# Performance work log

Hardware: AMD Instinct MI355X
Metric: run time of the kernel (lower is better)

Reference implementation:

```python
import jax, jax.numpy as jnp
import numpy as np

HIDDEN = 1024
HEADS = 16
HEAD_DIM = HIDDEN // HEADS  # 64
LOCAL = (128, 128)
ROPE_MAX_POS = LOCAL[0] + LOCAL[1]  # 256 (local attention branch)
ROPE_BASE = 10000.0


def make_rope_cache(max_len, dim, base):
    positions = jnp.arange(max_len, dtype=jnp.float32)
    theta = 1.0 / base ** (jnp.arange(0, dim, 2, dtype=jnp.float32) / dim)
    angles = jnp.einsum('i,j->ij', positions, theta)
    return jnp.stack([jnp.cos(angles), jnp.sin(angles)], axis=-1)  # (max_len, dim//2, 2)


def apply_rope(x, cache):
    # x: (B, S, H, D); cache: (max_pos, D//2, 2)
    S = x.shape[1]
    pos = jnp.arange(S) % cache.shape[0]
    rc = cache[pos][None, :, None, :, :]  # (1, S, 1, D//2, 2)
    xr = x.reshape(*x.shape[:-1], -1, 2)
    x0, x1 = xr[..., 0], xr[..., 1]
    c, s = rc[..., 0], rc[..., 1]
    out = jnp.stack([x0 * c - x1 * s, x1 * c + x0 * s], axis=-1)
    return out.reshape(x.shape)


def sliding_window_mask(S, window, dtype):
    rel = jnp.arange(S)[:, None] - jnp.arange(S)[None, :]
    inside = (rel >= -window[0]) & (rel <= window[1])
    return jnp.where(inside, jnp.zeros((), dtype), -jnp.inf)[None, None]  # (1,1,S,S)


def setup_inputs() -> dict:
    key = jax.random.key(0)
    k1, k2, k3, k4, k5 = jax.random.split(key, 5)
    B, S = 2, 2048
    hidden_states = jax.random.normal(k1, (B, S, HIDDEN), dtype=jnp.float32)
    Wqkv_kernel = jax.random.normal(k2, (HIDDEN, 3 * HIDDEN), dtype=jnp.float32) / np.sqrt(HIDDEN)
    Wqkv_bias = jnp.zeros((3 * HIDDEN,), dtype=jnp.float32)
    Wo_kernel = jax.random.normal(k3, (HIDDEN, HIDDEN), dtype=jnp.float32) / np.sqrt(HIDDEN)
    Wo_bias = jnp.zeros((HIDDEN,), dtype=jnp.float32)
    rope_cache = make_rope_cache(ROPE_MAX_POS, HEAD_DIM, ROPE_BASE)
    return {
        'hidden_states': hidden_states,
        'Wqkv_kernel': Wqkv_kernel,
        'Wqkv_bias': Wqkv_bias,
        'Wo_kernel': Wo_kernel,
        'Wo_bias': Wo_bias,
        'rope_cache': rope_cache,
    }


def reference(hidden_states, Wqkv_kernel, Wqkv_bias, Wo_kernel, Wo_bias, rope_cache):
    B, S, _ = hidden_states.shape
    qkv = hidden_states @ Wqkv_kernel + Wqkv_bias  # (B,S,3*HIDDEN)
    qkv = qkv.reshape(B, S, 3, HEADS, HEAD_DIM)
    q = qkv[:, :, 0]  # (B,S,H,D)
    k = qkv[:, :, 1]
    v = qkv[:, :, 2]
    q = apply_rope(q, rope_cache)
    k = apply_rope(k, rope_cache)
    # to (B,H,S,D)
    q = jnp.transpose(q, (0, 2, 1, 3))
    k = jnp.transpose(k, (0, 2, 1, 3))
    v = jnp.transpose(v, (0, 2, 1, 3))
    scale = jnp.sqrt(jnp.float32(HEAD_DIM))
    scores = jnp.einsum('bhqd,bhkd->bhqk', q, k) / scale
    mask = sliding_window_mask(S, LOCAL, scores.dtype)
    probs = jax.nn.softmax(scores + mask, axis=-1)
    out = jnp.einsum('bhqk,bhkd->bqhd', probs, v).reshape(B, S, HIDDEN)
    out = out @ Wo_kernel + Wo_bias
    return out
```

## Files before the change

### kernel.cpp

```cpp
#include <hip/hip_runtime.h>
#include <hip/hip_bf16.h>

typedef __bf16 bf16x8 __attribute__((ext_vector_type(8)));
typedef __bf16 bf16x4 __attribute__((ext_vector_type(4)));
typedef float f32x4 __attribute__((ext_vector_type(4)));

#define SLEN 2048
#define NHEADS 16
#define HDIM 64

__global__ __launch_bounds__(256) void cast_f32_bf16(const float* __restrict__ in,
                                                     __bf16* __restrict__ out, int n4) {
    int i = blockIdx.x * 256 + threadIdx.x;
    if (i < n4) {
        float4 v = reinterpret_cast<const float4*>(in)[i];
        bf16x4 o = { (__bf16)v.x, (__bf16)v.y, (__bf16)v.z, (__bf16)v.w };
        reinterpret_cast<bf16x4*>(out)[i] = o;
    }
}

__global__ __launch_bounds__(256) void transpose_cast(const float* __restrict__ W,
                                                      __bf16* __restrict__ Wt,
                                                      int K, int N) {
    __shared__ float tile[32][33];
    int n0 = blockIdx.x * 32, k0 = blockIdx.y * 32;
    int tx = threadIdx.x, ty = threadIdx.y;
    #pragma unroll
    for (int i = ty; i < 32; i += 8)
        tile[i][tx] = W[(size_t)(k0 + i) * N + n0 + tx];
    __syncthreads();
    #pragma unroll
    for (int i = ty; i < 32; i += 8)
        Wt[(size_t)(n0 + i) * K + k0 + tx] = (__bf16)tile[tx][i];
}

__global__ __launch_bounds__(256) void gemm_bt(const __bf16* __restrict__ A,
                                               const __bf16* __restrict__ Bt,
                                               const float* __restrict__ bias,
                                               float* __restrict__ Cf,
                                               __bf16* __restrict__ Cq,
                                               __bf16* __restrict__ Ck,
                                               __bf16* __restrict__ Cv,
                                               int M, int N, int K, int epi) {
    __shared__ __align__(16) __bf16 As[128 * 40];
    __shared__ __align__(16) __bf16 Bs[128 * 40];

    int nb = N >> 7;
    int bx = blockIdx.x % nb;
    int by = blockIdx.x / nb;
    int row0 = by * 128, col0 = bx * 128;

    int tid = threadIdx.x;
    int wave = tid >> 6, lane = tid & 63;
    int quad = lane >> 4, lrow = lane & 15;
    int wm = wave >> 1, wn = wave & 1;

    int r1 = tid >> 2;
    int kk = (tid & 3) * 8;
    const __bf16* Aptr = A + (size_t)(row0 + r1) * K + kk;
    const __bf16* Bptr = Bt + (size_t)(col0 + r1) * K + kk;

    f32x4 acc[4][4];
    f32x4 zero = {0.f, 0.f, 0.f, 0.f};
    #pragma unroll
    for (int i = 0; i < 4; i++)
        #pragma unroll
        for (int j = 0; j < 4; j++) acc[i][j] = zero;

    for (int k0 = 0; k0 < K; k0 += 32) {
        bf16x8 a0 = *reinterpret_cast<const bf16x8*>(Aptr + k0);
        bf16x8 a1 = *reinterpret_cast<const bf16x8*>(Aptr + (size_t)64 * K + k0);
        bf16x8 b0 = *reinterpret_cast<const bf16x8*>(Bptr + k0);
        bf16x8 b1 = *reinterpret_cast<const bf16x8*>(Bptr + (size_t)64 * K + k0);
        __syncthreads();
        *reinterpret_cast<bf16x8*>(&As[r1 * 40 + kk]) = a0;
        *reinterpret_cast<bf16x8*>(&As[(r1 + 64) * 40 + kk]) = a1;
        *reinterpret_cast<bf16x8*>(&Bs[r1 * 40 + kk]) = b0;
        *reinterpret_cast<bf16x8*>(&Bs[(r1 + 64) * 40 + kk]) = b1;
        __syncthreads();

        bf16x8 af[4], bfr[4];
        #pragma unroll
        for (int i = 0; i < 4; i++)
            af[i] = *reinterpret_cast<const bf16x8*>(&As[(wm * 64 + i * 16 + lrow) * 40 + quad * 8]);
        #pragma unroll
        for (int j = 0; j < 4; j++)
            bfr[j] = *reinterpret_cast<const bf16x8*>(&Bs[(wn * 64 + j * 16 + lrow) * 40 + quad * 8]);
        #pragma unroll
        for (int i = 0; i < 4; i++)
            #pragma unroll
            for (int j = 0; j < 4; j++)
                acc[i][j] = __builtin_amdgcn_mfma_f32_16x16x32_bf16(af[i], bfr[j], acc[i][j], 0, 0, 0);
    }

    #pragma unroll
    for (int i = 0; i < 4; i++) {
        int rowb = row0 + wm * 64 + i * 16 + quad * 4;
        #pragma unroll
        for (int j = 0; j < 4; j++) {
            int col = col0 + wn * 64 + j * 16 + lrow;
            float bsv = bias[col];
            #pragma unroll
            for (int r = 0; r < 4; r++) {
                int row = rowb + r;
                float v = acc[i][j][r] + bsv;
                if (epi == 0) {
                    Cf[(size_t)row * N + col] = v;
                } else {
                    int part = col >> 10;
                    int h = (col >> 6) & 15;
                    int d = col & 63;
                    int b = row >> 11;
                    int s = row & 2047;
                    __bf16* dst = (part == 0) ? Cq : ((part == 1) ? Ck : Cv);
                    dst[((size_t)(b * NHEADS + h) * SLEN + s) * HDIM + d] = (__bf16)v;
                }
            }
        }
    }
}

__global__ __launch_bounds__(256) void rope_kernel(__bf16* __restrict__ Q,
                                                   __bf16* __restrict__ K,
                                                   const float* __restrict__ rope) {
    int idx = blockIdx.x * 256 + threadIdx.x;
    int p = idx & 31;
    int s = (idx >> 5) & 2047;
    int bh = idx >> 16;
    size_t off = ((size_t)bh * SLEN + s) * HDIM + 2 * p;
    int pos = s & 255;
    float c = rope[(pos * 32 + p) * 2];
    float sn = rope[(pos * 32 + p) * 2 + 1];
    float q0 = (float)Q[off], q1 = (float)Q[off + 1];
    Q[off]     = (__bf16)(q0 * c - q1 * sn);
    Q[off + 1] = (__bf16)(q1 * c + q0 * sn);
    float k0 = (float)K[off], k1 = (float)K[off + 1];
    K[off]     = (__bf16)(k0 * c - k1 * sn);
    K[off + 1] = (__bf16)(k1 * c + k0 * sn);
}

__global__ __launch_bounds__(256) void attn_kernel(const __bf16* __restrict__ Q,
                                                   const __bf16* __restrict__ Kt,
                                                   const __bf16* __restrict__ V,
                                                   __bf16* __restrict__ O) {
    __shared__ __align__(16) __bf16 Vt[64][40];
    __shared__ __align__(16) __bf16 Pl[4][16][40];

    int qt = blockIdx.x & 31;
    int bh = blockIdx.x >> 5;
    int q0 = qt * 64;
    const __bf16* Qbh = Q + (size_t)bh * SLEN * HDIM;
    const __bf16* Kbh = Kt + (size_t)bh * SLEN * HDIM;
    const __bf16* Vbh = V + (size_t)bh * SLEN * HDIM;

    int tid = threadIdx.x;
    int wave = tid >> 6, lane = tid & 63;
    int quad = lane >> 4, lrow = lane & 15;
    int wq0 = q0 + wave * 16;

    bf16x8 qa0 = *reinterpret_cast<const bf16x8*>(Qbh + (size_t)(wq0 + lrow) * HDIM + quad * 8);
    bf16x8 qa1 = *reinterpret_cast<const bf16x8*>(Qbh + (size_t)(wq0 + lrow) * HDIM + 32 + quad * 8);

    f32x4 zero = {0.f, 0.f, 0.f, 0.f};
    f32x4 acc[4];
    #pragma unroll
    for (int t = 0; t < 4; t++) acc[t] = zero;
    float m_i[4], l_i[4];
    #pragma unroll
    for (int r = 0; r < 4; r++) { m_i[r] = -1e30f; l_i[r] = 0.f; }

    int kstart = q0 - 128; if (kstart < 0) kstart = 0;
    int kend = q0 + 63 + 128 + 1; if (kend > SLEN) kend = SLEN;

    for (int kc = kstart; kc < kend; kc += 32) {
        __syncthreads();
        {
            int keyl = tid >> 3;
            int db = (tid & 7) * 8;
            bf16x8 vv = *reinterpret_cast<const bf16x8*>(Vbh + (size_t)(kc + keyl) * HDIM + db);
            #pragma unroll
            for (int i = 0; i < 8; i++) Vt[db + i][keyl] = vv[i];
        }
        __syncthreads();

        f32x4 c0 = zero, c1 = zero;
        {
            const __bf16* krow0 = Kbh + (size_t)(kc + lrow) * HDIM;
            const __bf16* krow1 = Kbh + (size_t)(kc + 16 + lrow) * HDIM;
            bf16x8 kb0a = *reinterpret_cast<const bf16x8*>(krow0 + quad * 8);
            bf16x8 kb0b = *reinterpret_cast<const bf16x8*>(krow0 + 32 + quad * 8);
            bf16x8 kb1a = *reinterpret_cast<const bf16x8*>(krow1 + quad * 8);
            bf16x8 kb1b = *reinterpret_cast<const bf16x8*>(krow1 + 32 + quad * 8);
            c0 = __builtin_amdgcn_mfma_f32_16x16x32_bf16(qa0, kb0a, c0, 0, 0, 0);
            c0 = __builtin_amdgcn_mfma_f32_16x16x32_bf16(qa1, kb0b, c0, 0, 0, 0);
            c1 = __builtin_amdgcn_mfma_f32_16x16x32_bf16(qa0, kb1a, c1, 0, 0, 0);
            c1 = __builtin_amdgcn_mfma_f32_16x16x32_bf16(qa1, kb1b, c1, 0, 0, 0);
        }

        #pragma unroll
        for (int r = 0; r < 4; r++) {
            int q = wq0 + quad * 4 + r;
            int key0 = kc + lrow;
            int key1 = kc + 16 + lrow;
            bool v0 = (key0 >= q - 128) && (key0 <= q + 128);
            bool v1 = (key1 >= q - 128) && (key1 <= q + 128);
            float s0 = v0 ? c0[r] * 0.125f : -1e30f;
            float s1 = v1 ? c1[r] * 0.125f : -1e30f;
            float rm = fmaxf(s0, s1);
            #pragma unroll
            for (int off = 1; off < 16; off <<= 1) rm = fmaxf(rm, __shfl_xor(rm, off, 64));
            float mnew = fmaxf(m_i[r], rm);
            float alpha = __expf(m_i[r] - mnew);
            float p0 = v0 ? __expf(s0 - mnew) : 0.0f;
            float p1 = v1 ? __expf(s1 - mnew) : 0.0f;
            float rs = p0 + p1;
            #pragma unroll
            for (int off = 1; off < 16; off <<= 1) rs += __shfl_xor(rs, off, 64);
            l_i[r] = l_i[r] * alpha + rs;
            m_i[r] = mnew;
            #pragma unroll
            for (int t = 0; t < 4; t++) acc[t][r] *= alpha;
            Pl[wave][quad * 4 + r][lrow] = (__bf16)p0;
            Pl[wave][quad * 4 + r][16 + lrow] = (__bf16)p1;
        }
        asm volatile("s_waitcnt lgkmcnt(0)" ::: "memory");

        bf16x8 ap = *reinterpret_cast<const bf16x8*>(&Pl[wave][lrow][quad * 8]);
        #pragma unroll
        for (int t = 0; t < 4; t++) {
            bf16x8 bv = *reinterpret_cast<const bf16x8*>(&Vt[t * 16 + lrow][quad * 8]);
            acc[t] = __builtin_amdgcn_mfma_f32_16x16x32_bf16(ap, bv, acc[t], 0, 0, 0);
        }
    }

    int b = bh >> 4, h = bh & 15;
    #pragma unroll
    for (int r = 0; r < 4; r++) {
        int stok = q0 + wave * 16 + quad * 4 + r;
        float inv = 1.0f / l_i[r];
        size_t base = ((size_t)b * SLEN + stok) * 1024 + h * HDIM;
        #pragma unroll
        for (int t = 0; t < 4; t++) {
            O[base + t * 16 + lrow] = (__bf16)(acc[t][r] * inv);
        }
    }
}

extern "C" void kernel_launch(void* const* d_in, const int* in_sizes, int n_in,
                              void* d_out, int out_size, void* d_ws, size_t ws_size,
                              hipStream_t stream) {
    const float* hidden = (const float*)d_in[0];
    const float* Wqkv   = (const float*)d_in[1];
    const float* bqkv   = (const float*)d_in[2];
    const float* Wo     = (const float*)d_in[3];
    const float* bo     = (const float*)d_in[4];
    const float* rope   = (const float*)d_in[5];
    float* out = (float*)d_out;

    char* ws = (char*)d_ws;
    __bf16* A1  = (__bf16*)(ws);
    __bf16* Wt  = (__bf16*)(ws + 8388608);
    __bf16* Wot = (__bf16*)(ws + 14680064);
    __bf16* Qb  = (__bf16*)(ws + 16777216);
    __bf16* Kb  = (__bf16*)(ws + 25165824);
    __bf16* Vb  = (__bf16*)(ws + 33554432);
    __bf16* AO  = (__bf16*)(ws + 41943040);

    cast_f32_bf16<<<4096, 256, 0, stream>>>(hidden, A1, 1048576);
    transpose_cast<<<dim3(96, 32), dim3(32, 8), 0, stream>>>(Wqkv, Wt, 1024, 3072);
    transpose_cast<<<dim3(32, 32), dim3(32, 8), 0, stream>>>(Wo, Wot, 1024, 1024);

    gemm_bt<<<32 * 24, 256, 0, stream>>>(A1, Wt, bqkv, nullptr, Qb, Kb, Vb,
                                         4096, 3072, 1024, 1);
    rope_kernel<<<8192, 256, 0, stream>>>(Qb, Kb, rope);
    attn_kernel<<<2 * 16 * 32, 256, 0, stream>>>(Qb, Kb, Vb, AO);
    gemm_bt<<<32 * 8, 256, 0, stream>>>(AO, Wot, bo, out, nullptr, nullptr, nullptr,
                                        4096, 1024, 1024, 0);
}
```

Before: 205.6 us.

## Fuse RoPE into QKV GEMM epilogue, async LDS loads, widen attention key chunks

Removes the standalone RoPE kernel by applying the rotation in the QKV GEMM epilogue, using a lane shuffle to fetch the paired element. This saves a full read and write pass over Q and K. The GEMM now loads tiles with global_load_lds direct-to-LDS copies into an XOR-swizzled unpadded layout instead of staging through registers. The attention kernel processes 64 keys per iteration instead of 32, which halves the barrier and softmax-reduction overhead per key but raises register and LDS use.

```diff
diff --git a/kernel.cpp b/kernel.cpp
--- a/kernel.cpp
+++ b/kernel.cpp
@@ -8,6 +8,12 @@
 #define SLEN 2048
 #define NHEADS 16
 #define HDIM 64
+
+__device__ __forceinline__ void async_copy16(const __bf16* g, void* l) {
+    __builtin_amdgcn_global_load_lds(
+        (const __attribute__((address_space(1))) void*)g,
+        (__attribute__((address_space(3))) void*)l, 16, 0, 0);
+}
 
 __global__ __launch_bounds__(256) void cast_f32_bf16(const float* __restrict__ in,
                                                      __bf16* __restrict__ out, int n4) {
@@ -37,13 +43,14 @@
 __global__ __launch_bounds__(256) void gemm_bt(const __bf16* __restrict__ A,
                                                const __bf16* __restrict__ Bt,
                                                const float* __restrict__ bias,
+                                               const float* __restrict__ rope,
                                                float* __restrict__ Cf,
                                                __bf16* __restrict__ Cq,
                                                __bf16* __restrict__ Ck,
                                                __bf16* __restrict__ Cv,
                                                int M, int N, int K, int epi) {
-    __shared__ __align__(16) __bf16 As[128 * 40];
-    __shared__ __align__(16) __bf16 Bs[128 * 40];
+    __shared__ __align__(16) __bf16 As[128 * 32];
+    __shared__ __align__(16) __bf16 Bs[128 * 32];
 
     int nb = N >> 7;
     int bx = blockIdx.x % nb;
@@ -57,8 +64,11 @@
 
     int r1 = tid >> 2;
     int kk = (tid & 3) * 8;
-    const __bf16* Aptr = A + (size_t)(row0 + r1) * K + kk;
-    const __bf16* Bptr = Bt + (size_t)(col0 + r1) * K + kk;
+    int kg = kk ^ (((r1 >> 1) & 3) * 8);
+    const __bf16* Ap = A + (size_t)(row0 + r1) * K + kg;
+    const __bf16* Bp = Bt + (size_t)(col0 + r1) * K + kg;
+    char* as_lo = (char*)As + wave * 1024;
+    char* bs_lo = (char*)Bs + wave * 1024;
 
     f32x4 acc[4][4];
     f32x4 zero = {0.f, 0.f, 0.f, 0.f};
@@ -67,25 +77,23 @@
         #pragma unroll
         for (int j = 0; j < 4; j++) acc[i][j] = zero;
 
+    int sA = (quad ^ ((lrow >> 1) & 3)) * 8;
+
     for (int k0 = 0; k0 < K; k0 += 32) {
-        bf16x8 a0 = *reinterpret_cast<const bf16x8*>(Aptr + k0);
-        bf16x8 a1 = *reinterpret_cast<const bf16x8*>(Aptr + (size_t)64 * K + k0);
-        bf16x8 b0 = *reinterpret_cast<const bf16x8*>(Bptr + k0);
-        bf16x8 b1 = *reinterpret_cast<const bf16x8*>(Bptr + (size_t)64 * K + k0);
-        __syncthreads();
-        *reinterpret_cast<bf16x8*>(&As[r1 * 40 + kk]) = a0;
-        *reinterpret_cast<bf16x8*>(&As[(r1 + 64) * 40 + kk]) = a1;
-        *reinterpret_cast<bf16x8*>(&Bs[r1 * 40 + kk]) = b0;
-        *reinterpret_cast<bf16x8*>(&Bs[(r1 + 64) * 40 + kk]) = b1;
+        __syncthreads();
+        async_copy16(Ap + k0, as_lo);
+        async_copy16(Ap + (size_t)64 * K + k0, as_lo + 4096);
+        async_copy16(Bp + k0, bs_lo);
+        async_copy16(Bp + (size_t)64 * K + k0, bs_lo + 4096);
         __syncthreads();
 
         bf16x8 af[4], bfr[4];
         #pragma unroll
         for (int i = 0; i < 4; i++)
-            af[i] = *reinterpret_cast<const bf16x8*>(&As[(wm * 64 + i * 16 + lrow) * 40 + quad * 8]);
+            af[i] = *reinterpret_cast<const bf16x8*>(&As[(wm * 64 + i * 16 + lrow) * 32 + sA]);
         #pragma unroll
         for (int j = 0; j < 4; j++)
-            bfr[j] = *reinterpret_cast<const bf16x8*>(&Bs[(wn * 64 + j * 16 + lrow) * 40 + quad * 8]);
+            bfr[j] = *reinterpret_cast<const bf16x8*>(&Bs[(wn * 64 + j * 16 + lrow) * 32 + sA]);
         #pragma unroll
         for (int i = 0; i < 4; i++)
             #pragma unroll
@@ -93,6 +101,8 @@
                 acc[i][j] = __builtin_amdgcn_mfma_f32_16x16x32_bf16(af[i], bfr[j], acc[i][j], 0, 0, 0);
     }
 
+    int part = col0 >> 10;
+    bool do_rope = (epi == 1) && (part < 2);
     #pragma unroll
     for (int i = 0; i < 4; i++) {
         int rowb = row0 + wm * 64 + i * 16 + quad * 4;
@@ -100,16 +110,23 @@
         for (int j = 0; j < 4; j++) {
             int col = col0 + wn * 64 + j * 16 + lrow;
             float bsv = bias[col];
+            int d = col & 63;
             #pragma unroll
             for (int r = 0; r < 4; r++) {
                 int row = rowb + r;
                 float v = acc[i][j][r] + bsv;
+                if (do_rope) {
+                    int pos = row & 255;
+                    int p = d >> 1;
+                    float c  = rope[(pos * 32 + p) * 2];
+                    float sn = rope[(pos * 32 + p) * 2 + 1];
+                    float other = __shfl_xor(v, 1, 64);
+                    v = (d & 1) ? fmaf(v, c, other * sn) : fmaf(v, c, -other * sn);
+                }
                 if (epi == 0) {
                     Cf[(size_t)row * N + col] = v;
                 } else {
-                    int part = col >> 10;
                     int h = (col >> 6) & 15;
-                    int d = col & 63;
                     int b = row >> 11;
                     int s = row & 2047;
                     __bf16* dst = (part == 0) ? Cq : ((part == 1) ? Ck : Cv);
@@ -120,31 +137,12 @@
     }
 }
 
-__global__ __launch_bounds__(256) void rope_kernel(__bf16* __restrict__ Q,
-                                                   __bf16* __restrict__ K,
-                                                   const float* __restrict__ rope) {
-    int idx = blockIdx.x * 256 + threadIdx.x;
-    int p = idx & 31;
-    int s = (idx >> 5) & 2047;
-    int bh = idx >> 16;
-    size_t off = ((size_t)bh * SLEN + s) * HDIM + 2 * p;
-    int pos = s & 255;
-    float c = rope[(pos * 32 + p) * 2];
-    float sn = rope[(pos * 32 + p) * 2 + 1];
-    float q0 = (float)Q[off], q1 = (float)Q[off + 1];
-    Q[off]     = (__bf16)(q0 * c - q1 * sn);
-    Q[off + 1] = (__bf16)(q1 * c + q0 * sn);
-    float k0 = (float)K[off], k1 = (float)K[off + 1];
-    K[off]     = (__bf16)(k0 * c - k1 * sn);
-    K[off + 1] = (__bf16)(k1 * c + k0 * sn);
-}
-
 __global__ __launch_bounds__(256) void attn_kernel(const __bf16* __restrict__ Q,
                                                    const __bf16* __restrict__ Kt,
                                                    const __bf16* __restrict__ V,
                                                    __bf16* __restrict__ O) {
-    __shared__ __align__(16) __bf16 Vt[64][40];
-    __shared__ __align__(16) __bf16 Pl[4][16][40];
+    __shared__ __align__(16) __bf16 Vt[64][72];
+    __shared__ __align__(16) __bf16 Pl[4][16][72];
 
     int qt = blockIdx.x & 31;
     int bh = blockIdx.x >> 5;
@@ -172,64 +170,75 @@
     int kstart = q0 - 128; if (kstart < 0) kstart = 0;
     int kend = q0 + 63 + 128 + 1; if (kend > SLEN) kend = SLEN;
 
-    for (int kc = kstart; kc < kend; kc += 32) {
+    for (int kc = kstart; kc < kend; kc += 64) {
         __syncthreads();
         {
-            int keyl = tid >> 3;
-            int db = (tid & 7) * 8;
-            bf16x8 vv = *reinterpret_cast<const bf16x8*>(Vbh + (size_t)(kc + keyl) * HDIM + db);
-            #pragma unroll
-            for (int i = 0; i < 8; i++) Vt[db + i][keyl] = vv[i];
-        }
-        __syncthreads();
-
-        f32x4 c0 = zero, c1 = zero;
-        {
-            const __bf16* krow0 = Kbh + (size_t)(kc + lrow) * HDIM;
-            const __bf16* krow1 = Kbh + (size_t)(kc + 16 + lrow) * HDIM;
-            bf16x8 kb0a = *reinterpret_cast<const bf16x8*>(krow0 + quad * 8);
-            bf16x8 kb0b = *reinterpret_cast<const bf16x8*>(krow0 + 32 + quad * 8);
-            bf16x8 kb1a = *reinterpret_cast<const bf16x8*>(krow1 + quad * 8);
-            bf16x8 kb1b = *reinterpret_cast<const bf16x8*>(krow1 + 32 + quad * 8);
-            c0 = __builtin_amdgcn_mfma_f32_16x16x32_bf16(qa0, kb0a, c0, 0, 0, 0);
-            c0 = __builtin_amdgcn_mfma_f32_16x16x32_bf16(qa1, kb0b, c0, 0, 0, 0);
-            c1 = __builtin_amdgcn_mfma_f32_16x16x32_bf16(qa0, kb1a, c1, 0, 0, 0);
-            c1 = __builtin_amdgcn_mfma_f32_16x16x32_bf16(qa1, kb1b, c1, 0, 0, 0);
+            int keyl = tid >> 2;
+            int db = (tid & 3) * 16;
+            const __bf16* vp = Vbh + (size_t)(kc + keyl) * HDIM + db;
+            bf16x8 v0 = *reinterpret_cast<const bf16x8*>(vp);
+            bf16x8 v1 = *reinterpret_cast<const bf16x8*>(vp + 8);
+            #pragma unroll
+            for (int i = 0; i < 8; i++) {
+                Vt[db + i][keyl] = v0[i];
+                Vt[db + 8 + i][keyl] = v1[i];
+            }
+        }
+        __syncthreads();
+
+        f32x4 cs[4];
+        #pragma unroll
+        for (int sub = 0; sub < 4; sub++) {
+            cs[sub] = zero;
+            const __bf16* krow = Kbh + (size_t)(kc + sub * 16 + lrow) * HDIM;
+            bf16x8 kba = *reinterpret_cast<const bf16x8*>(krow + quad * 8);
+            bf16x8 kbb = *reinterpret_cast<const bf16x8*>(krow + 32 + quad * 8);
+            cs[sub] = __builtin_amdgcn_mfma_f32_16x16x32_bf16(qa0, kba, cs[sub], 0, 0, 0);
+            cs[sub] = __builtin_amdgcn_mfma_f32_16x16x32_bf16(qa1, kbb, cs[sub], 0, 0, 0);
         }
 
         #pragma unroll
         for (int r = 0; r < 4; r++) {
             int q = wq0 + quad * 4 + r;
-            int key0 = kc + lrow;
-            int key1 = kc + 16 + lrow;
-            bool v0 = (key0 >= q - 128) && (key0 <= q + 128);
-            bool v1 = (key1 >= q - 128) && (key1 <= q + 128);
-            float s0 = v0 ? c0[r] * 0.125f : -1e30f;
-            float s1 = v1 ? c1[r] * 0.125f : -1e30f;
-            float rm = fmaxf(s0, s1);
+            float sc[4];
+            bool vd[4];
+            #pragma unroll
+            for (int sub = 0; sub < 4; sub++) {
+                int key = kc + sub * 16 + lrow;
+                vd[sub] = (key >= q - 128) && (key <= q + 128);
+                sc[sub] = vd[sub] ? cs[sub][r] * 0.125f : -1e30f;
+            }
+            float rm = fmaxf(fmaxf(sc[0], sc[1]), fmaxf(sc[2], sc[3]));
             #pragma unroll
             for (int off = 1; off < 16; off <<= 1) rm = fmaxf(rm, __shfl_xor(rm, off, 64));
             float mnew = fmaxf(m_i[r], rm);
             float alpha = __expf(m_i[r] - mnew);
-            float p0 = v0 ? __expf(s0 - mnew) : 0.0f;
-            float p1 = v1 ? __expf(s1 - mnew) : 0.0f;
-            float rs = p0 + p1;
+            float p[4], rs = 0.f;
+            #pragma unroll
+            for (int sub = 0; sub < 4; sub++) {
+                p[sub] = vd[sub] ? __expf(sc[sub] - mnew) : 0.0f;
+                rs += p[sub];
+            }
             #pragma unroll
             for (int off = 1; off < 16; off <<= 1) rs += __shfl_xor(rs, off, 64);
             l_i[r] = l_i[r] * alpha + rs;
             m_i[r] = mnew;
             #pragma unroll
             for (int t = 0; t < 4; t++) acc[t][r] *= alpha;
-            Pl[wave][quad * 4 + r][lrow] = (__bf16)p0;
-            Pl[wave][quad * 4 + r][16 + lrow] = (__bf16)p1;
+            #pragma unroll
+            for (int sub = 0; sub < 4; sub++)
+                Pl[wave][quad * 4 + r][sub * 16 + lrow] = (__bf16)p[sub];
         }
         asm volatile("s_waitcnt lgkmcnt(0)" ::: "memory");
 
-        bf16x8 ap = *reinterpret_cast<const bf16x8*>(&Pl[wave][lrow][quad * 8]);
+        bf16x8 ap0 = *reinterpret_cast<const bf16x8*>(&Pl[wave][lrow][quad * 8]);
+        bf16x8 ap1 = *reinterpret_cast<const bf16x8*>(&Pl[wave][lrow][32 + quad * 8]);
         #pragma unroll
         for (int t = 0; t < 4; t++) {
-            bf16x8 bv = *reinterpret_cast<const bf16x8*>(&Vt[t * 16 + lrow][quad * 8]);
-            acc[t] = __builtin_amdgcn_mfma_f32_16x16x32_bf16(ap, bv, acc[t], 0, 0, 0);
+            bf16x8 bv0 = *reinterpret_cast<const bf16x8*>(&Vt[t * 16 + lrow][quad * 8]);
+            bf16x8 bv1 = *reinterpret_cast<const bf16x8*>(&Vt[t * 16 + lrow][32 + quad * 8]);
+            acc[t] = __builtin_amdgcn_mfma_f32_16x16x32_bf16(ap0, bv0, acc[t], 0, 0, 0);
+            acc[t] = __builtin_amdgcn_mfma_f32_16x16x32_bf16(ap1, bv1, acc[t], 0, 0, 0);
         }
     }
 
@@ -270,10 +279,9 @@
     transpose_cast<<<dim3(96, 32), dim3(32, 8), 0, stream>>>(Wqkv, Wt, 1024, 3072);
     transpose_cast<<<dim3(32, 32), dim3(32, 8), 0, stream>>>(Wo, Wot, 1024, 1024);
 
-    gemm_bt<<<32 * 24, 256, 0, stream>>>(A1, Wt, bqkv, nullptr, Qb, Kb, Vb,
+    gemm_bt<<<32 * 24, 256, 0, stream>>>(A1, Wt, bqkv, rope, nullptr, Qb, Kb, Vb,
                                          4096, 3072, 1024, 1);
-    rope_kernel<<<8192, 256, 0, stream>>>(Qb, Kb, rope);
     attn_kernel<<<2 * 16 * 32, 256, 0, stream>>>(Qb, Kb, Vb, AO);
-    gemm_bt<<<32 * 8, 256, 0, stream>>>(AO, Wot, bo, out, nullptr, nullptr, nullptr,
+    gemm_bt<<<32 * 8, 256, 0, stream>>>(AO, Wot, bo, rope, out, nullptr, nullptr, nullptr,
                                         4096, 1024, 1024, 0);
 }
```

Result: no change. 207.5 us (+0.9%).
